# Kernel tuning notes

Measured on AMD Instinct MI355X. Metric: run time of the kernel, lower is better.

Reference implementation:

```python
import jax, jax.numpy as jnp
import numpy as np
from jax import lax

# SoftDTW constants from module-level `sdtw = SoftDTW(use_cuda=False, gamma=0.01, warp=134.4)`
GAMMA = 0.01
WARP = 134.4
BIG = 1e9        # finite stand-in for inf boundary (grad-safe; exp(-BIG/GAMMA) underflows to exactly 0)
MASK_INF = 100000.0
# loss alphas (config.loss.*)
KL_ALPHA = 1.0
KL_FWD_ALPHA = 1.0
GEN_ALPHA = 1.0
GEN_E2E_ALPHA = 1.0
FEAT_ALPHA = 2.0
DUR_ALPHA = 1.0
PITCH_ALPHA = 1.0
MEL_ALPHA = 45.0


def soft_dtw(D):
    """Soft-DTW with warp penalty (NaturalSpeech variant).
    D: [b, n, m] cost matrix. Returns [b] soft-DTW values R[n-1, m-1] of
      R[i,j] = D[i,j] + softmin_gamma(R[i-1,j-1], R[i-1,j]+warp, R[i,j-1]+warp)
    computed over anti-diagonals (wavefront) so each scan step is vectorized.
    """
    b, n, m = D.shape
    K = n + m - 1
    i_idx = jnp.arange(n)
    ks = jnp.arange(K)

    def pack(k):  # pack anti-diagonal k of D, indexed by row i
        j = k - i_idx
        v = (j >= 0) & (j < m)
        return jnp.where(v[None, :], D[:, i_idx, jnp.clip(j, 0, m - 1)], 0.0), v

    Dd, Vd = jax.vmap(pack)(ks)  # Dd: [K, b, n], Vd: [K, n]
    init = jnp.full((b, n), BIG, dtype=D.dtype)

    def step(carry, xs):
        r1, r2 = carry  # previous diag (k-1) and diag (k-2), indexed by row i
        dk, v, k = xs
        # diagonal predecessor (i-1, j-1): on diag k-2 at row i-1; (−1,−1) boundary = 0 only at k==0
        first = jnp.where(k == 0, 0.0, BIG).astype(D.dtype)
        r_diag = jnp.concatenate([jnp.broadcast_to(first, (b, 1)), r2[:, :-1]], axis=1)
        # up predecessor (i-1, j): diag k-1, row i-1
        r_up = jnp.concatenate([jnp.full((b, 1), BIG, dtype=D.dtype), r1[:, :-1]], axis=1)
        # left predecessor (i, j-1): diag k-1, row i
        stacked = jnp.stack([-r_diag, -(r_up + WARP), -(r1 + WARP)]) / GAMMA
        smin = -GAMMA * jax.nn.logsumexp(stacked, axis=0)
        r_new = jnp.where(v[None, :], dk + smin, BIG)
        return (r_new, r1), None

    (rf, _), _ = lax.scan(step, (init, init), (Dd, Vd, ks))
    return rf[:, n - 1]  # cell (n-1, m-1) lies on the last diagonal at row n-1


def kl_matrix(z, lq, m, lp):
    """kl[b,p,q] = sum_h lp - lq - 0.5 + 0.5*(z-m)^2*exp(-2lp); rows (m,lp) [b,h,P], cols (z,lq) [b,h,Q]."""
    h = m.shape[1]
    a = jnp.exp(-2.0 * lp)  # [b,h,P]
    quad = (jnp.einsum('bhp,bhq->bpq', a, z * z)
            - 2.0 * jnp.einsum('bhp,bhq->bpq', a * m, z)
            + jnp.sum(a * m * m, axis=1)[:, :, None])
    return jnp.sum(lp, axis=1)[:, :, None] - jnp.sum(lq, axis=1)[:, None, :] - 0.5 * h + 0.5 * quad


def kl_loss_sdtw(z, lq, m, lp, p_mask, q_mask):
    kl = kl_matrix(z, lq, m, lp)
    kl = jnp.pad(kl, ((0, 0), (0, 1), (0, 1)))
    pmf = jnp.pad(p_mask.astype(jnp.float32), ((0, 0), (0, 1)))
    qmf = jnp.pad(q_mask.astype(jnp.float32), ((0, 0), (0, 1)))
    pb, qb = pmf.astype(bool), qmf.astype(bool)
    kl = jnp.where(pb[:, :, None] ^ qb[:, None, :], MASK_INF, kl)
    kl = jnp.where((~pb[:, :, None]) & (~qb[:, None, :]), 0.0, kl)
    return soft_dtw(kl).sum() / pmf.sum()


def setup_inputs() -> dict:
    key = jax.random.key(0)
    ks = jax.random.split(key, 16)
    B, H, T = 8, 192, 400
    d = {
        'mel_slice': jax.random.normal(ks[0], (B, 80, T), jnp.float32),
        'mel_slice_hat': jax.random.normal(ks[1], (B, 80, T), jnp.float32),
        'scores_disc_fake': jax.random.normal(ks[2], (6, B, T), jnp.float32),
        'scores_disc_fake_e2e': jax.random.normal(ks[3], (6, B, T), jnp.float32),
        'feats_disc_real': jax.random.normal(ks[4], (30, B, 128, T), jnp.float32),
        'feats_disc_fake': jax.random.normal(ks[5], (30, B, 128, T), jnp.float32),
        'duration_loss': jax.random.uniform(ks[6], (1,), jnp.float32),
        'pitch_loss': jax.random.uniform(ks[7], (1,), jnp.float32),
        'z_p': jax.random.normal(ks[8], (B, H, T), jnp.float32),
        'm_p': jax.random.normal(ks[9], (B, H, T), jnp.float32),
        'logs_p': jax.random.normal(ks[10], (B, H, T), jnp.float32),
        'z_q': jax.random.normal(ks[11], (B, H, T), jnp.float32),
        'm_q': jax.random.normal(ks[12], (B, H, T), jnp.float32),
        'logs_q': jax.random.normal(ks[13], (B, H, T), jnp.float32),
        'p_mask': jnp.ones((B, T), jnp.int32),
        'z_mask': jnp.ones((B, T), jnp.int32),
    }
    return d


def reference(mel_slice, mel_slice_hat, scores_disc_fake, scores_disc_fake_e2e,
              feats_disc_real, feats_disc_fake, duration_loss, pitch_loss,
              z_p, m_p, logs_p, z_q, m_q, logs_q, p_mask, z_mask):
    # generator losses: sum over discriminator maps of mean((1 - s)^2)
    loss_gen = jnp.mean((1.0 - scores_disc_fake) ** 2, axis=(1, 2)).sum() * GEN_ALPHA
    loss_gen_e2e = jnp.mean((1.0 - scores_disc_fake_e2e) ** 2, axis=(1, 2)).sum() * GEN_E2E_ALPHA
    # feature matching: 2 * sum over feature maps of mean|real.detach() - fake|
    fr = lax.stop_gradient(feats_disc_real)
    loss_fm = 2.0 * jnp.mean(jnp.abs(fr - feats_disc_fake), axis=(1, 2, 3)).sum() * FEAT_ALPHA
    loss_mel = jnp.mean(jnp.abs(mel_slice - mel_slice_hat)) * MEL_ALPHA
    loss_dur = jnp.sum(duration_loss) * DUR_ALPHA
    loss_pitch = jnp.sum(pitch_loss) * PITCH_ALPHA
    # soft-DTW KL (both directions)
    loss_kl = kl_loss_sdtw(z_p, logs_q, m_p, logs_p, p_mask, z_mask) * KL_ALPHA
    loss_kl_fwd = kl_loss_sdtw(z_q, logs_p, m_q, logs_q, z_mask, p_mask) * KL_FWD_ALPHA
    total = loss_gen + loss_gen_e2e + loss_fm + loss_mel + loss_dur + loss_pitch + loss_kl + loss_kl_fwd
    return jnp.stack([loss_gen, loss_gen_e2e, loss_fm, loss_mel, loss_dur,
                      loss_pitch, loss_kl, loss_kl_fwd, total])
```

## Files before the change

### kernel.cpp

```cpp
#include <hip/hip_runtime.h>
#include <math.h>

#define BIGV      1e9f
#define WARP_PEN  134.4f
#define MASK_INF_C 100000.0f

#define B   8
#define H   192
#define T   400
#define NP  401
#define NPROB 16
#define NTIL 51
#define TSLAB (NTIL*NTIL*64)
#define SBLOCKS 768

typedef float f32x4 __attribute__((ext_vector_type(4)));

#define SLOT_OFF 16
#define LSP_OFF 160
#define LSQ_OFF (160 + B*T)
#define C1P_OFF (160 + 2*B*T)
#define C1Q_OFF (160 + 3*B*T)
#define DMAT_OFF (160 + 4*B*T)

__device__ __forceinline__ float wave_shr1(float src, float fill) {
    int r = __builtin_amdgcn_update_dpp(__float_as_int(fill), __float_as_int(src),
                                        0x138 , 0xf, 0xf, false);
    return __int_as_float(r);
}

__global__ __launch_bounds__(256)
void colsum(const float* __restrict__ logs_p, const float* __restrict__ m_p,
            const float* __restrict__ logs_q, const float* __restrict__ m_q,
            float* __restrict__ ws) {
    int b = blockIdx.x / 7;
    int lane = threadIdx.x & 63;
    int hq = threadIdx.x >> 6;
    int t = (blockIdx.x % 7) * 64 + lane;
    __shared__ float part[4][4][64];
    float lp_s = 0.f, lq_s = 0.f, c1p = 0.f, c1q = 0.f;
    if (t < T) {
        int base = b*H*T + hq*48*T + t;
        const float* LP = logs_p + base;
        const float* MP = m_p   + base;
        const float* LQ = logs_q + base;
        const float* MQ = m_q   + base;
#pragma unroll 4
        for (int h = 0; h < 48; ++h) {
            float lp = LP[h*T], mp = MP[h*T];
            float lq = LQ[h*T], mq = MQ[h*T];
            lp_s += lp;
            lq_s += lq;
            c1p += __expf(-2.f*lp) * mp * mp;
            c1q += __expf(-2.f*lq) * mq * mq;
        }
    }
    part[hq][0][lane] = lp_s;
    part[hq][1][lane] = lq_s;
    part[hq][2][lane] = c1p;
    part[hq][3][lane] = c1q;
    __syncthreads();
    if (hq == 0 && t < T) {
        float a0 = part[0][0][lane] + part[1][0][lane] + part[2][0][lane] + part[3][0][lane];
        float a1 = part[0][1][lane] + part[1][1][lane] + part[2][1][lane] + part[3][1][lane];
        float a2 = part[0][2][lane] + part[1][2][lane] + part[2][2][lane] + part[3][2][lane];
        float a3 = part[0][3][lane] + part[1][3][lane] + part[2][3][lane] + part[3][3][lane];
        ws[LSP_OFF + b*T + t] = a0;
        ws[LSQ_OFF + b*T + t] = a1;
        ws[C1P_OFF + b*T + t] = a2;
        ws[C1Q_OFF + b*T + t] = a3;
    }
}

#define TILE 64
#define KH 32
__global__ __launch_bounds__(256)
void kl_gemm(const float* __restrict__ z_p, const float* __restrict__ m_p,
             const float* __restrict__ logs_p,
             const float* __restrict__ z_q, const float* __restrict__ m_q,
             const float* __restrict__ logs_q,
             const int* __restrict__ p_mask, const int* __restrict__ z_mask,
             float* __restrict__ ws) {
    int prob = blockIdx.y;
    int dir = prob >> 3, b = prob & 7;
    int tp = blockIdx.x / 7, tq = blockIdx.x % 7;
    int p0 = tp * TILE, q0 = tq * TILE;

    const float* lp_arr = dir ? logs_q : logs_p;
    const float* m_arr  = dir ? m_q    : m_p;
    const float* z_arr  = dir ? z_q    : z_p;
    const float* Lp = ws + (dir ? LSQ_OFF : LSP_OFF) + b*T;
    const float* Lq = ws + (dir ? LSP_OFF : LSQ_OFF) + b*T;
    const float* C1 = ws + (dir ? C1Q_OFF : C1P_OFF) + b*T;
    const int* rmask = dir ? z_mask : p_mask;
    const int* cmask = dir ? p_mask : z_mask;

    __shared__ __align__(16) float As [KH][TILE+4];
    __shared__ __align__(16) float AMs[KH][TILE+4];
    __shared__ __align__(16) float Zs [KH][TILE+4];
    __shared__ __align__(16) float Z2s[KH][TILE+4];

    int tid = threadIdx.x;
    int tx = tid & 15, ty = tid >> 4;

    float acc1[4][4] = {{0.f}}, acc2[4][4] = {{0.f}};

    const float* lpB = lp_arr + b*H*T;
    const float* mB  = m_arr  + b*H*T;
    const float* zB  = z_arr  + b*H*T;

    for (int h0 = 0; h0 < H; h0 += KH) {
        for (int e = tid; e < KH*TILE; e += 256) {
            int hh = e >> 6, tt = e & 63;
            int pg = p0 + tt; if (pg > T-1) pg = T-1;
            int qg = q0 + tt; if (qg > T-1) qg = T-1;
            float lp = lpB[(h0+hh)*T + pg];
            float mv = mB [(h0+hh)*T + pg];
            float a  = __expf(-2.f*lp);
            As [hh][tt] = a;
            AMs[hh][tt] = a * mv;
            float zv = zB[(h0+hh)*T + qg];
            Zs [hh][tt] = zv;
            Z2s[hh][tt] = zv * zv;
        }
        __syncthreads();
#pragma unroll 8
        for (int hh = 0; hh < KH; ++hh) {
            const float4 av  = *(const float4*)(&As [hh][ty*4]);
            const float4 amv = *(const float4*)(&AMs[hh][ty*4]);
            const float4 zv  = *(const float4*)(&Zs [hh][tx*4]);
            const float4 z2v = *(const float4*)(&Z2s[hh][tx*4]);
            const float pa[4]  = {av.x, av.y, av.z, av.w};
            const float pam[4] = {amv.x, amv.y, amv.z, amv.w};
            const float qz[4]  = {zv.x, zv.y, zv.z, zv.w};
            const float qz2[4] = {z2v.x, z2v.y, z2v.z, z2v.w};
#pragma unroll
            for (int ii = 0; ii < 4; ++ii)
#pragma unroll
                for (int jj = 0; jj < 4; ++jj) {
                    acc1[ii][jj] = fmaf(pa[ii],  qz2[jj], acc1[ii][jj]);
                    acc2[ii][jj] = fmaf(pam[ii], qz[jj],  acc2[ii][jj]);
                }
        }
        __syncthreads();
    }

    float* Dm = ws + DMAT_OFF + (size_t)prob * TSLAB;
#pragma unroll
    for (int ii = 0; ii < 4; ++ii) {
        int p = p0 + ty*4 + ii;
        if (p > NP-1) continue;
        int pc = p < T ? p : T-1;
        float lpv = Lp[pc];
        float c1v = C1[pc];
        bool pmv = (p < T) && (rmask[b*T + p] != 0);
#pragma unroll
        for (int jj = 0; jj < 4; ++jj) {
            int q = q0 + tx*4 + jj;
            if (q > NP-1) continue;
            int qc = q < T ? q : T-1;
            bool qmv = (q < T) && (cmask[b*T + q] != 0);
            float val = lpv - Lq[qc] - 0.5f*(float)H
                      + 0.5f*(acc1[ii][jj] - 2.f*acc2[ii][jj] + c1v);
            float outv = (pmv != qmv) ? MASK_INF_C : ((!pmv && !qmv) ? 0.f : val);
            int off = ((p >> 3) * NTIL + (q >> 3)) * 64 + (p & 7) * 8 + (q & 7);
            Dm[off] = outv;
        }
    }
}

__global__ __launch_bounds__(256, 1)
void fused_dtw_scalar(const float* __restrict__ Dd, float* __restrict__ acc,
                      const float* __restrict__ mel, const float* __restrict__ melh,
                      const float* __restrict__ sg,  const float* __restrict__ se,
                      const float* __restrict__ fr,  const float* __restrict__ ff,
                      const int* __restrict__ pm,    const int* __restrict__ zm) {
    if (blockIdx.x < NPROB) {
        if (threadIdx.x >= 64) return;
        int prob = blockIdx.x;
        int lane = threadIdx.x;
        int Ieff = lane < (NTIL-1) ? lane : (NTIL-1);
        const float* tbase = Dd + (size_t)prob * TSLAB + Ieff * ((NTIL-1) * 64);

        float brow[8], browW[8], rightraw[8], rightW[8];
        float brold = BIGV, v00 = BIGV;
#pragma unroll
        for (int t = 0; t < 8; ++t) {
            brow[t] = BIGV; browW[t] = BIGV; rightraw[t] = BIGV; rightW[t] = BIGV;
        }

        f32x4 bufA[16], bufB[16];
#pragma unroll
        for (int t = 0; t < 16; ++t) bufA[t] = *(const f32x4*)(tbase + t * 4);

#define TILE_STEP(CUR, NXT, SVAL, DO_LOAD)                                    \
    {                                                                          \
        const int s_ = (SVAL);                                                 \
        bool jz = (s_ == lane);                                    \
        float brnew = brow[7];                                                 \
          \
        _Pragma("unroll")                                                      \
        for (int c = 0; c < 8; ++c) {                                          \
            brow[c] = wave_shr1(brow[c], BIGV);                                \
            browW[c] = brow[c] + WARP_PEN;                                     \
        }                                                                      \
        float corner = wave_shr1(brold, BIGV);                                 \
        if (jz) corner = (lane == 0) ? 0.f : BIGV;                             \
        if (DO_LOAD) {                                                         \
            const float* np_ = tbase + (s_ + 1) * 64;                          \
            _Pragma("unroll")                                                  \
            for (int t = 0; t < 16; ++t) NXT[t] = *(const f32x4*)(np_ + t*4);  \
            __builtin_amdgcn_sched_barrier(0);  \
        }                                                                      \
        float dprev = corner;                                                  \
        _Pragma("unroll")                                                      \
        for (int r = 0; r < 8; ++r) {                                          \
            float leftW = jz ? BIGV : rightW[r];                               \
            float dnextrow = jz ? BIGV : rightraw[r];    \
            float diag = dprev;                                                \
            _Pragma("unroll")                                                  \
            for (int c = 0; c < 8; ++c) {                                      \
                float dv = CUR[r*2 + (c>>2)][c & 3];                           \
                float v = fminf(fminf(diag, browW[c]), leftW) + dv;            \
                if (r == 0 && c == 0) v00 = v;                                 \
                float t_ = brow[c];        \
                brow[c] = v;                                                   \
                float vW = v + WARP_PEN;                                       \
                browW[c] = vW;                                                 \
                leftW = vW;                                                    \
                diag = t_;                                                     \
            }                                                                  \
            rightraw[r] = brow[7];                                             \
            rightW[r]   = browW[7];                                            \
            dprev = dnextrow;                                                  \
        }                                                                      \
        brold = brnew;                                                         \
    }

        for (int sb = 0; sb < 100; sb += 2) {
            TILE_STEP(bufA, bufB, sb,     1)
            TILE_STEP(bufB, bufA, sb + 1, 1)
        }
        TILE_STEP(bufA, bufB, 100, 0)
#undef TILE_STEP

        if (lane == NTIL-1) atomicAdd(&acc[6 + (prob >> 3)], v00);
    } else {
        float s0 = 0.f, s1 = 0.f, s2 = 0.f, s3 = 0.f, s4 = 0.f, s5 = 0.f;
        int tid = (blockIdx.x - NPROB) * 256 + threadIdx.x;
        const int stride = SBLOCKS * 256;

        const float4* fr4 = (const float4*)fr;
        const float4* ff4 = (const float4*)ff;
        for (int i = tid; i < 3072000; i += stride) {
            float4 a = fr4[i], b = ff4[i];
            s2 += fabsf(a.x - b.x) + fabsf(a.y - b.y) + fabsf(a.z - b.z) + fabsf(a.w - b.w);
        }
        const float4* m4 = (const float4*)mel;
        const float4* mh4 = (const float4*)melh;
        for (int i = tid; i < 64000; i += stride) {
            float4 a = m4[i], b = mh4[i];
            s3 += fabsf(a.x - b.x) + fabsf(a.y - b.y) + fabsf(a.z - b.z) + fabsf(a.w - b.w);
        }
        const float4* g4 = (const float4*)sg;
        const float4* e4 = (const float4*)se;
        for (int i = tid; i < 4800; i += stride) {
            float4 a = g4[i], b = e4[i];
            float gx = 1.f - a.x, gy = 1.f - a.y, gz = 1.f - a.z, gw = 1.f - a.w;
            s0 += gx*gx + gy*gy + gz*gz + gw*gw;
            float hx = 1.f - b.x, hy = 1.f - b.y, hz = 1.f - b.z, hw = 1.f - b.w;
            s1 += hx*hx + hy*hy + hz*hz + hw*hw;
        }
        for (int i = tid; i < B*T; i += stride) {
            s4 += (float)pm[i];
            s5 += (float)zm[i];
        }
        for (int off = 32; off > 0; off >>= 1) {
            s0 += __shfl_down(s0, off); s1 += __shfl_down(s1, off);
            s2 += __shfl_down(s2, off); s3 += __shfl_down(s3, off);
            s4 += __shfl_down(s4, off); s5 += __shfl_down(s5, off);
        }
        __shared__ float red[4][8];
        int wid = threadIdx.x >> 6;
        if ((threadIdx.x & 63) == 0) {
            red[wid][0] = s0; red[wid][1] = s1; red[wid][2] = s2;
            red[wid][3] = s3; red[wid][4] = s4; red[wid][5] = s5;
        }
        __syncthreads();
        if (threadIdx.x == 0) {
            float t0 = 0.f, t1 = 0.f, t2 = 0.f, t3 = 0.f, t4 = 0.f, t5 = 0.f;
#pragma unroll
            for (int w = 0; w < 4; ++w) {
                t0 += red[w][0]; t1 += red[w][1]; t2 += red[w][2];
                t3 += red[w][3]; t4 += red[w][4]; t5 += red[w][5];
            }
            float* slot = acc + SLOT_OFF + (blockIdx.x & 7) * 16;
            atomicAdd(&slot[0], t0); atomicAdd(&slot[1], t1);
            atomicAdd(&slot[2], t2); atomicAdd(&slot[3], t3);
            atomicAdd(&slot[4], t4); atomicAdd(&slot[5], t5);
        }
    }
}

__global__ void finalize(const float* __restrict__ acc,
                         const float* __restrict__ dur,
                         const float* __restrict__ pit,
                         float* __restrict__ out) {
    if (threadIdx.x != 0 || blockIdx.x != 0) return;
    float t[6] = {0.f, 0.f, 0.f, 0.f, 0.f, 0.f};
    for (int s = 0; s < 8; ++s)
        for (int c = 0; c < 6; ++c)
            t[c] += acc[SLOT_OFF + s*16 + c];
    float gen  = t[0] / 3200.f;
    float e2e  = t[1] / 3200.f;
    float fm   = 4.f * t[2] / 409600.f;
    float melv = 45.f * t[3] / 256000.f;
    float d    = dur[0];
    float p    = pit[0];
    float kl   = acc[6] / t[4];
    float klf  = acc[7] / t[5];
    out[0] = gen; out[1] = e2e; out[2] = fm; out[3] = melv;
    out[4] = d;   out[5] = p;   out[6] = kl; out[7] = klf;
    out[8] = gen + e2e + fm + melv + d + p + kl + klf;
}

extern "C" void kernel_launch(void* const* d_in, const int* in_sizes, int n_in,
                              void* d_out, int out_size, void* d_ws, size_t ws_size,
                              hipStream_t stream) {
    const float* mel    = (const float*)d_in[0];
    const float* melh   = (const float*)d_in[1];
    const float* sg     = (const float*)d_in[2];
    const float* se     = (const float*)d_in[3];
    const float* fr     = (const float*)d_in[4];
    const float* ff     = (const float*)d_in[5];
    const float* dur    = (const float*)d_in[6];
    const float* pit    = (const float*)d_in[7];
    const float* z_p    = (const float*)d_in[8];
    const float* m_p    = (const float*)d_in[9];
    const float* logs_p = (const float*)d_in[10];
    const float* z_q    = (const float*)d_in[11];
    const float* m_q    = (const float*)d_in[12];
    const float* logs_q = (const float*)d_in[13];
    const int*   p_mask = (const int*)d_in[14];
    const int*   z_mask = (const int*)d_in[15];
    float* ws  = (float*)d_ws;
    float* out = (float*)d_out;

    hipMemsetAsync(ws, 0, 160 * sizeof(float), stream);
    colsum<<<B*7, 256, 0, stream>>>(logs_p, m_p, logs_q, m_q, ws);
    kl_gemm<<<dim3(49, NPROB), 256, 0, stream>>>(z_p, m_p, logs_p, z_q, m_q, logs_q,
                                                 p_mask, z_mask, ws);
    fused_dtw_scalar<<<NPROB + SBLOCKS, 256, 0, stream>>>(ws + DMAT_OFF, ws,
                                                          mel, melh, sg, se, fr, ff,
                                                          p_mask, z_mask);
    finalize<<<1, 64, 0, stream>>>(ws, dur, pit, out);
}
```

Measured before the change: 142.3 us.

## Store DTW cost tiles by anti-diagonal and stream them via async global-to-LDS loads

The cost matrix is rewritten in an anti-diagonal-packed tile layout, so each wavefront step's tiles are contiguous and the loads coalesce across lanes. The DTW wave now prefetches diagonals two steps ahead into a triple-buffered LDS ring using global_load_lds, with manual vmcnt waits, in place of register double-buffering. This aims to hide global load latency on the serial critical path and to free registers. It adds 48KB of LDS to every block, including the reduction blocks, and drops the occupancy-1 launch bound, which may reduce occupancy for the reduction blocks. It also relies on hand-counted waitcnt correctness.

New measurement: 166.3 us. +16.8%, slower.

```diff
diff --git a/kernel.cpp b/kernel.cpp
--- a/kernel.cpp
+++ b/kernel.cpp
@@ -10,8 +10,7 @@
 #define T   400
 #define NP  401
 #define NPROB 16
-#define NTIL 51
-#define TSLAB (NTIL*NTIL*64)
+#define TSLAB 166464
 #define SBLOCKS 768
 
 typedef float f32x4 __attribute__((ext_vector_type(4)));
@@ -22,6 +21,12 @@
 #define C1P_OFF (160 + 2*B*T)
 #define C1Q_OFF (160 + 3*B*T)
 #define DMAT_OFF (160 + 4*B*T)
+
+__device__ __forceinline__ int diag_len(int s) { return (s <= 50) ? s + 1 : 101 - s; }
+__device__ __forceinline__ int diag_i0 (int s) { return (s <= 50) ? 0 : s - 50; }
+__device__ __forceinline__ int diag_Cs (int s) {
+    return (s <= 51) ? s * (s + 1) / 2 : 2601 - (101 - s) * (102 - s) / 2;
+}
 
 __device__ __forceinline__ float wave_shr1(float src, float fill) {
     int r = __builtin_amdgcn_update_dpp(__float_as_int(fill), __float_as_int(src),
@@ -163,24 +168,28 @@
             float val = lpv - Lq[qc] - 0.5f*(float)H
                       + 0.5f*(acc1[ii][jj] - 2.f*acc2[ii][jj] + c1v);
             float outv = (pmv != qmv) ? MASK_INF_C : ((!pmv && !qmv) ? 0.f : val);
-            int off = ((p >> 3) * NTIL + (q >> 3)) * 64 + (p & 7) * 8 + (q & 7);
+            int I8 = p >> 3, J8 = q >> 3, sdg = I8 + J8;
+            int len = diag_len(sdg), i0 = diag_i0(sdg), Cs = diag_Cs(sdg);
+            int k = (p & 7) * 2 + ((q & 7) >> 2);
+            int off = Cs*64 + (k*len + (I8 - i0))*4 + (q & 3);
             Dm[off] = outv;
         }
     }
 }
 
-__global__ __launch_bounds__(256, 1)
+__global__ __launch_bounds__(256)
 void fused_dtw_scalar(const float* __restrict__ Dd, float* __restrict__ acc,
                       const float* __restrict__ mel, const float* __restrict__ melh,
                       const float* __restrict__ sg,  const float* __restrict__ se,
                       const float* __restrict__ fr,  const float* __restrict__ ff,
                       const int* __restrict__ pm,    const int* __restrict__ zm) {
+    __shared__ float dlds[3 * 4096];
+    __shared__ float red[4][8];
     if (blockIdx.x < NPROB) {
         if (threadIdx.x >= 64) return;
         int prob = blockIdx.x;
         int lane = threadIdx.x;
-        int Ieff = lane < (NTIL-1) ? lane : (NTIL-1);
-        const float* tbase = Dd + (size_t)prob * TSLAB + Ieff * ((NTIL-1) * 64);
+        const float* Dp = Dd + (size_t)prob * TSLAB;
 
         float brow[8], browW[8], rightraw[8], rightW[8];
         float brold = BIGV, v00 = BIGV;
@@ -189,16 +198,26 @@
             brow[t] = BIGV; browW[t] = BIGV; rightraw[t] = BIGV; rightW[t] = BIGV;
         }
 
-        f32x4 bufA[16], bufB[16];
-#pragma unroll
-        for (int t = 0; t < 16; ++t) bufA[t] = *(const f32x4*)(tbase + t * 4);
-
-#define TILE_STEP(CUR, NXT, SVAL, DO_LOAD)                                    \
+        auto issue_diag = [&](int sp, int ldsoff) {
+            if (sp > 100) sp = 100;
+            int len = diag_len(sp), i0 = diag_i0(sp), Cs = diag_Cs(sp);
+            int pos = lane - i0;
+            pos = pos < 0 ? 0 : pos;
+            pos = pos > len - 1 ? len - 1 : pos;
+            const float* srcb = Dp + Cs*64 + pos*4;
+            int str = len * 4;
+#pragma unroll
+            for (int k = 0; k < 16; ++k)
+                __builtin_amdgcn_global_load_lds(srcb + k*str, &dlds[ldsoff + k*256], 16, 0, 0);
+        };
+
+#define TILE_STEP(CUROFF, NXTOFF, SVAL)                                       \
     {                                                                          \
         const int s_ = (SVAL);                                                 \
+        issue_diag(s_ + 2, NXTOFF);                                            \
+        asm volatile("s_waitcnt vmcnt(32)" ::: "memory");                      \
         bool jz = (s_ == lane);                                    \
         float brnew = brow[7];                                                 \
-          \
         _Pragma("unroll")                                                      \
         for (int c = 0; c < 8; ++c) {                                          \
             brow[c] = wave_shr1(brow[c], BIGV);                                \
@@ -206,29 +225,28 @@
         }                                                                      \
         float corner = wave_shr1(brold, BIGV);                                 \
         if (jz) corner = (lane == 0) ? 0.f : BIGV;                             \
-        if (DO_LOAD) {                                                         \
-            const float* np_ = tbase + (s_ + 1) * 64;                          \
-            _Pragma("unroll")                                                  \
-            for (int t = 0; t < 16; ++t) NXT[t] = *(const f32x4*)(np_ + t*4);  \
-            __builtin_amdgcn_sched_barrier(0);  \
-        }                                                                      \
         float dprev = corner;                                                  \
         _Pragma("unroll")                                                      \
         for (int r = 0; r < 8; ++r) {                                          \
             float leftW = jz ? BIGV : rightW[r];                               \
-            float dnextrow = jz ? BIGV : rightraw[r];    \
+            float dnextrow = jz ? BIGV : rightraw[r];                          \
             float diag = dprev;                                                \
             _Pragma("unroll")                                                  \
-            for (int c = 0; c < 8; ++c) {                                      \
-                float dv = CUR[r*2 + (c>>2)][c & 3];                           \
-                float v = fminf(fminf(diag, browW[c]), leftW) + dv;            \
-                if (r == 0 && c == 0) v00 = v;                                 \
-                float t_ = brow[c];        \
-                brow[c] = v;                                                   \
-                float vW = v + WARP_PEN;                                       \
-                browW[c] = vW;                                                 \
-                leftW = vW;                                                    \
-                diag = t_;                                                     \
+            for (int ch = 0; ch < 2; ++ch) {                                   \
+                const int k_ = r*2 + ch;                                       \
+                f32x4 dvv = *(const f32x4*)&dlds[CUROFF + k_*256 + lane*4];    \
+                _Pragma("unroll")                                              \
+                for (int cc = 0; cc < 4; ++cc) {                               \
+                    const int c = ch*4 + cc;                                   \
+                    float v = fminf(fminf(diag, browW[c]), leftW) + dvv[cc];   \
+                    if (r == 0 && c == 0) v00 = v;                             \
+                    float t_ = brow[c];                                        \
+                    brow[c] = v;                                               \
+                    float vW = v + WARP_PEN;                                   \
+                    browW[c] = vW;                                             \
+                    leftW = vW;                                                \
+                    diag = t_;                                                 \
+                }                                                              \
             }                                                                  \
             rightraw[r] = brow[7];                                             \
             rightW[r]   = browW[7];                                            \
@@ -237,14 +255,20 @@
         brold = brnew;                                                         \
     }
 
-        for (int sb = 0; sb < 100; sb += 2) {
-            TILE_STEP(bufA, bufB, sb,     1)
-            TILE_STEP(bufB, bufA, sb + 1, 1)
-        }
-        TILE_STEP(bufA, bufB, 100, 0)
+        issue_diag(0, 0);
+        issue_diag(1, 4096);
+
+        for (int sb = 0; sb < 99; sb += 3) {
+            TILE_STEP(0,    8192, sb)
+            TILE_STEP(4096, 0,    sb + 1)
+            TILE_STEP(8192, 4096, sb + 2)
+        }
+        TILE_STEP(0,    8192, 99)
+        TILE_STEP(4096, 0,    100)
 #undef TILE_STEP
-
-        if (lane == NTIL-1) atomicAdd(&acc[6 + (prob >> 3)], v00);
+        asm volatile("s_waitcnt vmcnt(0)" ::: "memory");
+
+        if (lane == 50) atomicAdd(&acc[6 + (prob >> 3)], v00);
     } else {
         float s0 = 0.f, s1 = 0.f, s2 = 0.f, s3 = 0.f, s4 = 0.f, s5 = 0.f;
         int tid = (blockIdx.x - NPROB) * 256 + threadIdx.x;
@@ -280,7 +304,6 @@
             s2 += __shfl_down(s2, off); s3 += __shfl_down(s3, off);
             s4 += __shfl_down(s4, off); s5 += __shfl_down(s5, off);
         }
-        __shared__ float red[4][8];
         int wid = threadIdx.x >> 6;
         if ((threadIdx.x & 63) == 0) {
             red[wid][0] = s0; red[wid][1] = s1; red[wid][2] = s2;
```
